# Performance work log

Hardware: AMD Instinct MI355X
Metric: run time of the kernel (lower is better)

Reference implementation:

```python
import jax, jax.numpy as jnp
import numpy as np

N_NODES = 100000


def gcn_conv(x, W, b, row, col, n):
    """PyG GCNConv: linear transform, then symmetric-normalized aggregation
    with self-loops (add_self_loops=True, normalize=True, bias=True)."""
    h = x @ W  # [N, F_out]
    e_ones = jnp.ones(row.shape[0], dtype=x.dtype)
    # in-degree of target nodes, +1 for the implicit self-loop
    deg = jax.ops.segment_sum(e_ones, col, num_segments=n) + 1.0
    dinv = jax.lax.rsqrt(deg)  # deg >= 1 always
    norm = dinv[row] * dinv[col]  # [E]
    msg = h[row] * norm[:, None]  # gather + scale, [E, F_out]
    agg = jax.ops.segment_sum(msg, col, num_segments=n)  # scatter-add to targets
    agg = agg + h * (dinv * dinv)[:, None]  # self-loop contribution
    return agg + b


def setup_inputs() -> dict:
    key = jax.random.key(0)
    k1, k2, k3, k4 = jax.random.split(key, 4)
    F_in, F_hid, F_out = 512, 64, 40
    E = 1_600_000
    x = jax.random.normal(k1, (N_NODES, F_in), dtype=jnp.float32)
    edge_index = jax.random.randint(k2, (2, E), 0, N_NODES, dtype=jnp.int64)
    # Glorot-ish scaling for weights
    W1 = jax.random.normal(k3, (F_in, F_hid), dtype=jnp.float32) * (1.0 / np.sqrt(F_in))
    W2 = jax.random.normal(k4, (F_hid, F_out), dtype=jnp.float32) * (1.0 / np.sqrt(F_hid))
    b1 = jnp.zeros((F_hid,), dtype=jnp.float32)
    b2 = jnp.zeros((F_out,), dtype=jnp.float32)
    return {"x": x, "edge_index": edge_index, "W1": W1, "b1": b1, "W2": W2, "b2": b2}


def reference(x, edge_index, W1, b1, W2, b2):
    n = x.shape[0]
    row, col = edge_index[0], edge_index[1]
    h = jax.nn.relu(gcn_conv(x, W1, b1, row, col, n))
    # dropout is identity in eval mode (training=False)
    h = gcn_conv(h, W2, b2, row, col, n)
    return jax.nn.log_softmax(h, axis=1)
```

## Files before the change

### kernel.cpp

```cpp
#include <hip/hip_runtime.h>
#include <math.h>


#define FIN 512
#define FHID 64
#define FOUT 40

#define BSH 8
#define BN 256
#define BCAP 5120
#define EPW 4096

typedef __attribute__((ext_vector_type(8))) short short8;
typedef __attribute__((ext_vector_type(4))) float f32x4;
typedef unsigned short ushort_t;
typedef unsigned int uint_t;

__device__ __forceinline__ ushort_t bf16_rn(float f) {
    union { float f; uint_t u; } v; v.f = f;
    uint_t r = v.u + 0x7FFF + ((v.u >> 16) & 1);
    return (ushort_t)(r >> 16);
}
__device__ __forceinline__ uint_t pack_bf16(float a, float b) {
    return (uint_t)bf16_rn(a) | ((uint_t)bf16_rn(b) << 16);
}
__device__ __forceinline__ float bf16_to_f(ushort_t u) {
    union { uint_t i; float f; } t; t.i = ((uint_t)u) << 16; return t.f;
}
__device__ __forceinline__ void acc8(float* acc, uint4 g, float nm) {
    acc[0] = fmaf(__uint_as_float(g.x << 16), nm, acc[0]);
    acc[1] = fmaf(__uint_as_float(g.x & 0xFFFF0000u), nm, acc[1]);
    acc[2] = fmaf(__uint_as_float(g.y << 16), nm, acc[2]);
    acc[3] = fmaf(__uint_as_float(g.y & 0xFFFF0000u), nm, acc[3]);
    acc[4] = fmaf(__uint_as_float(g.z << 16), nm, acc[4]);
    acc[5] = fmaf(__uint_as_float(g.z & 0xFFFF0000u), nm, acc[5]);
    acc[6] = fmaf(__uint_as_float(g.w << 16), nm, acc[6]);
    acc[7] = fmaf(__uint_as_float(g.w & 0xFFFF0000u), nm, acc[7]);
}

__global__ __launch_bounds__(256) void bucket_scatter_kernel(
    const int* __restrict__ row, const int* __restrict__ col,
    int* __restrict__ gcur, uint_t* __restrict__ stage, int E) {
    __shared__ uint_t cnt[512];
    __shared__ uint_t base[512];
    int tid = threadIdx.x;
    cnt[tid] = 0; cnt[tid + 256] = 0;
    __syncthreads();
    int e0 = blockIdx.x * EPW;
    int creg[16];
#pragma unroll
    for (int it = 0; it < 16; ++it) {
        int e = e0 + it * 256 + tid;
        creg[it] = (e < E) ? col[e] : -1;
        if (e < E) atomicAdd(&cnt[((uint_t)creg[it]) >> BSH], 1u);
    }
    __syncthreads();
    uint_t c0 = cnt[tid], c1 = cnt[tid + 256];
    base[tid] = c0 ? (uint_t)atomicAdd(&gcur[tid], (int)c0) : 0u;
    base[tid + 256] = c1 ? (uint_t)atomicAdd(&gcur[tid + 256], (int)c1) : 0u;
    __syncthreads();
    cnt[tid] = 0; cnt[tid + 256] = 0;
    __syncthreads();
#pragma unroll
    for (int it = 0; it < 16; ++it) {
        int e = e0 + it * 256 + tid;
        if (e < E) {
            int c = creg[it];
            int r = row[e];
            int b = c >> BSH;
            uint_t slot = base[b] + atomicAdd(&cnt[b], 1u);
            stage[(size_t)b * BCAP + slot] = ((uint_t)r << BSH) | (uint_t)(c & (BN - 1));
        }
    }
}

__global__ void scan2_kernel(int* __restrict__ bsums, int nb) {
    __shared__ int tmp[512];
    int tid = threadIdx.x;
    int v = (tid < nb) ? bsums[tid] : 0;
    tmp[tid] = v;
    __syncthreads();
    for (int off = 1; off < 512; off <<= 1) {
        int t = (tid >= off) ? tmp[tid - off] : 0;
        __syncthreads();
        tmp[tid] += t;
        __syncthreads();
    }
    if (tid < nb) bsums[tid] = tmp[tid] - v;
}

__global__ __launch_bounds__(256) void bucket_place_kernel(
    const int* __restrict__ gcur, const uint_t* __restrict__ stage,
    int* __restrict__ sSrc, int* __restrict__ deg, float* __restrict__ dinv,
    int* __restrict__ offs, int n) {
    __shared__ int lcnt[256];
    __shared__ int ltmp[256];
    __shared__ int lpos[256];
    int b = blockIdx.x, tid = threadIdx.x;
    int nodeBase = b << BSH;
    int bucketBase = gcur[b];
    int cnt = gcur[b + 1] - bucketBase;
    lcnt[tid] = 0;
    __syncthreads();
    const uint_t* sp = &stage[(size_t)b * BCAP];
    for (int i = tid; i < cnt; i += 256)
        atomicAdd(&lcnt[sp[i] & (BN - 1)], 1);
    __syncthreads();
    int v = lcnt[tid];
    ltmp[tid] = v;
    __syncthreads();
    for (int off = 1; off < 256; off <<= 1) {
        int t = (tid >= off) ? ltmp[tid - off] : 0;
        __syncthreads();
        ltmp[tid] += t;
        __syncthreads();
    }
    int gofs = bucketBase + ltmp[tid] - v;
    int node = nodeBase + tid;
    if (node < n) {
        deg[node] = v;
        dinv[node] = rsqrtf((float)v + 1.0f);
        offs[node] = gofs;
    }
    lpos[tid] = gofs;
    __syncthreads();
    for (int i = tid; i < cnt; i += 256) {
        uint_t w = sp[i];
        int pos = atomicAdd(&lpos[w & (BN - 1)], 1);
        sSrc[pos] = (int)(w >> BSH);
    }
}

__global__ void wprep_kernel(const float* __restrict__ W1, const float* __restrict__ W2,
                             ushort_t* __restrict__ Wt,
                             ushort_t* __restrict__ w2hi, ushort_t* __restrict__ w2lo) {
    int idx = blockIdx.x * 256 + threadIdx.x;
    if (idx < 32768) {
        int nrow = idx >> 9;
        int k = idx & 511;
        Wt[idx] = bf16_rn(W1[k * 64 + nrow]);
    } else if (idx < 32768 + 3072) {
        int i = idx - 32768;
        int j = i >> 6, k = i & 63;
        float w = (j < FOUT) ? W2[k * FOUT + j] : 0.f;
        ushort_t h = bf16_rn(w);
        w2hi[i] = h;
        w2lo[i] = bf16_rn(w - bf16_to_f(h));
    }
}

#define LDA 72
#define LDB 72
__global__ __launch_bounds__(256) void gemm1_kernel(
    const float* __restrict__ x, const ushort_t* __restrict__ Wt,
    ushort_t* __restrict__ h1b, int n) {
    __shared__ ushort_t lA[128 * LDA];
    __shared__ ushort_t lB[64 * LDB];

    int tid = threadIdx.x;
    int wave = tid >> 6, lane = tid & 63;
    int quad = lane >> 4, m16 = lane & 15;
    int node0 = blockIdx.x * 128;

    int r0 = tid >> 4, k4 = tid & 15;
    int nr0 = tid >> 3, seg = tid & 7;

    f32x4 zero = {0.f, 0.f, 0.f, 0.f};
    f32x4 acc[2][4];
#pragma unroll
    for (int mt = 0; mt < 2; ++mt)
#pragma unroll
        for (int nt = 0; nt < 4; ++nt) acc[mt][nt] = zero;

    float4 ra[8];
    uint4 rb[2];

#pragma unroll
    for (int i = 0; i < 8; ++i) {
        int node = node0 + r0 + i * 16;
        float4 v = make_float4(0.f, 0.f, 0.f, 0.f);
        if (node < n) v = *reinterpret_cast<const float4*>(&x[(size_t)node * FIN + k4 * 4]);
        ra[i] = v;
    }
#pragma unroll
    for (int i = 0; i < 2; ++i)
        rb[i] = *reinterpret_cast<const uint4*>(&Wt[(size_t)(nr0 + i * 32) * FIN + seg * 8]);

    for (int c = 0; c < 8; ++c) {
#pragma unroll
        for (int i = 0; i < 8; ++i)
            *reinterpret_cast<uint2*>(&lA[(r0 + i * 16) * LDA + k4 * 4]) =
                make_uint2(pack_bf16(ra[i].x, ra[i].y), pack_bf16(ra[i].z, ra[i].w));
#pragma unroll
        for (int i = 0; i < 2; ++i)
            *reinterpret_cast<uint4*>(&lB[(nr0 + i * 32) * LDB + seg * 8]) = rb[i];
        __syncthreads();

        if (c < 7) {
            int kc = (c + 1) * 64;
#pragma unroll
            for (int i = 0; i < 8; ++i) {
                int node = node0 + r0 + i * 16;
                float4 v = make_float4(0.f, 0.f, 0.f, 0.f);
                if (node < n)
                    v = *reinterpret_cast<const float4*>(&x[(size_t)node * FIN + kc + k4 * 4]);
                ra[i] = v;
            }
#pragma unroll
            for (int i = 0; i < 2; ++i)
                rb[i] = *reinterpret_cast<const uint4*>(
                    &Wt[(size_t)(nr0 + i * 32) * FIN + kc + seg * 8]);
        }

#pragma unroll
        for (int kk = 0; kk < 2; ++kk) {
            short8 a[2], b[4];
#pragma unroll
            for (int mt = 0; mt < 2; ++mt)
                a[mt] = *reinterpret_cast<const short8*>(
                    &lA[(wave * 32 + mt * 16 + m16) * LDA + kk * 32 + quad * 8]);
#pragma unroll
            for (int nt = 0; nt < 4; ++nt)
                b[nt] = *reinterpret_cast<const short8*>(
                    &lB[(nt * 16 + m16) * LDB + kk * 32 + quad * 8]);
#pragma unroll
            for (int mt = 0; mt < 2; ++mt)
#pragma unroll
                for (int nt = 0; nt < 4; ++nt)
                    acc[mt][nt] = __builtin_amdgcn_mfma_f32_16x16x32_bf16(
                        a[mt], b[nt], acc[mt][nt], 0, 0, 0);
        }
        __syncthreads();
    }

#pragma unroll
    for (int mt = 0; mt < 2; ++mt) {
#pragma unroll
        for (int reg = 0; reg < 4; ++reg) {
            int node = node0 + wave * 32 + mt * 16 + quad * 4 + reg;
            if (node < n) {
#pragma unroll
                for (int nt = 0; nt < 4; ++nt)
                    h1b[(size_t)node * 64 + nt * 16 + m16] = bf16_rn(acc[mt][nt][reg]);
            }
        }
    }
}

template <int MODE>
__global__ __launch_bounds__(256) void agg_kernel(
    const int* __restrict__ offs, const int* __restrict__ deg,
    const int* __restrict__ sSrc, const ushort_t* __restrict__ src,
    const float* __restrict__ dinv, const float* __restrict__ b1,
    ushort_t* __restrict__ dst, int n) {
    __shared__ float lacc[4][8 * 68];
    __shared__ float lb1[64];
    int tid = threadIdx.x;
    if (MODE == 0 && tid < 64) lb1[tid] = b1[tid];

    int wv = tid >> 6, lane = tid & 63;
    int e8 = lane >> 3, c = lane & 7;
    int node = blockIdx.x * 4 + wv;
    bool valid = node < n;
    int start = valid ? offs[node] : 0;
    int cnt = valid ? deg[node] : 0;

    float acc[8];
#pragma unroll
    for (int j = 0; j < 8; ++j) acc[j] = 0.f;

    for (int base = 0; base < cnt; base += 32) {
        int i0 = base + e8, i1 = i0 + 8, i2 = i0 + 16, i3 = i0 + 24;
        int s0 = (i0 < cnt) ? sSrc[start + i0] : 0;
        int s1 = (i1 < cnt) ? sSrc[start + i1] : 0;
        int s2 = (i2 < cnt) ? sSrc[start + i2] : 0;
        int s3 = (i3 < cnt) ? sSrc[start + i3] : 0;
        float nm0 = (i0 < cnt) ? dinv[s0] : 0.f;
        float nm1 = (i1 < cnt) ? dinv[s1] : 0.f;
        float nm2 = (i2 < cnt) ? dinv[s2] : 0.f;
        float nm3 = (i3 < cnt) ? dinv[s3] : 0.f;
        uint4 g0 = *reinterpret_cast<const uint4*>(&src[(size_t)s0 * 64 + c * 8]);
        uint4 g1 = *reinterpret_cast<const uint4*>(&src[(size_t)s1 * 64 + c * 8]);
        uint4 g2 = *reinterpret_cast<const uint4*>(&src[(size_t)s2 * 64 + c * 8]);
        uint4 g3 = *reinterpret_cast<const uint4*>(&src[(size_t)s3 * 64 + c * 8]);
        acc8(acc, g0, nm0);
        acc8(acc, g1, nm1);
        acc8(acc, g2, nm2);
        acc8(acc, g3, nm3);
    }

    {
        float* lw = &lacc[wv][e8 * 68 + c * 8];
        *reinterpret_cast<float4*>(lw) = make_float4(acc[0], acc[1], acc[2], acc[3]);
        *reinterpret_cast<float4*>(lw + 4) = make_float4(acc[4], acc[5], acc[6], acc[7]);
    }
    __syncthreads();

    if (valid) {
        float s = 0.f;
#pragma unroll
        for (int g = 0; g < 8; ++g) s += lacc[wv][g * 68 + lane];
        float di = dinv[node];
        float self = bf16_to_f(src[(size_t)node * 64 + lane]) * di;
        float v = (s + self) * di;
        if (MODE == 0) v = fmaxf(v + lb1[lane], 0.f);
        dst[(size_t)node * 64 + lane] = bf16_rn(v);
    }
}

#define LDC 72
__global__ __launch_bounds__(256) void gemm2sm_kernel(
    const ushort_t* __restrict__ A, const ushort_t* __restrict__ w2hi,
    const ushort_t* __restrict__ w2lo, const float* __restrict__ b2,
    float* __restrict__ out, int n) {
    __shared__ ushort_t lA[128 * LDC];
    __shared__ ushort_t lBh[48 * LDC];
    __shared__ ushort_t lBl[48 * LDC];

    int tid = threadIdx.x;
    int wave = tid >> 6, lane = tid & 63;
    int quad = lane >> 4, m16 = lane & 15;
    int node0 = blockIdx.x * 128;

    {
        int r = tid & 127, part = tid >> 7;
        int node = node0 + r;
        uint4 z = make_uint4(0u, 0u, 0u, 0u);
        const uint4* sp = reinterpret_cast<const uint4*>(&A[(size_t)node * 64 + part * 32]);
#pragma unroll
        for (int i = 0; i < 4; ++i) {
            uint4 v = (node < n) ? sp[i] : z;
            *reinterpret_cast<uint4*>(&lA[r * LDC + part * 32 + i * 8]) = v;
        }
    }
    for (int i = tid; i < 384; i += 256) {
        int row = i >> 3, seg = i & 7;
        *reinterpret_cast<uint4*>(&lBh[row * LDC + seg * 8]) =
            reinterpret_cast<const uint4*>(w2hi)[i];
        *reinterpret_cast<uint4*>(&lBl[row * LDC + seg * 8]) =
            reinterpret_cast<const uint4*>(w2lo)[i];
    }
    float rb2_0 = b2[m16];
    float rb2_1 = b2[16 + m16];
    float rb2_2 = (m16 < 8) ? b2[32 + m16] : 0.f;
    __syncthreads();

    f32x4 zero = {0.f, 0.f, 0.f, 0.f};
    f32x4 acc[2][3];
#pragma unroll
    for (int mt = 0; mt < 2; ++mt)
#pragma unroll
        for (int nt = 0; nt < 3; ++nt) acc[mt][nt] = zero;

#pragma unroll
    for (int kk = 0; kk < 2; ++kk) {
        short8 a[2], bh[3], bl[3];
#pragma unroll
        for (int mt = 0; mt < 2; ++mt)
            a[mt] = *reinterpret_cast<const short8*>(
                &lA[(wave * 32 + mt * 16 + m16) * LDC + kk * 32 + quad * 8]);
#pragma unroll
        for (int nt = 0; nt < 3; ++nt) {
            bh[nt] = *reinterpret_cast<const short8*>(
                &lBh[(nt * 16 + m16) * LDC + kk * 32 + quad * 8]);
            bl[nt] = *reinterpret_cast<const short8*>(
                &lBl[(nt * 16 + m16) * LDC + kk * 32 + quad * 8]);
        }
#pragma unroll
        for (int mt = 0; mt < 2; ++mt)
#pragma unroll
            for (int nt = 0; nt < 3; ++nt) {
                acc[mt][nt] = __builtin_amdgcn_mfma_f32_16x16x32_bf16(
                    a[mt], bh[nt], acc[mt][nt], 0, 0, 0);
                acc[mt][nt] = __builtin_amdgcn_mfma_f32_16x16x32_bf16(
                    a[mt], bl[nt], acc[mt][nt], 0, 0, 0);
            }
    }

    bool c2 = (m16 < 8);
#pragma unroll
    for (int mt = 0; mt < 2; ++mt) {
#pragma unroll
        for (int reg = 0; reg < 4; ++reg) {
            int node = node0 + wave * 32 + mt * 16 + quad * 4 + reg;
            float r0 = acc[mt][0][reg] + rb2_0;
            float r1 = acc[mt][1][reg] + rb2_1;
            float r2 = acc[mt][2][reg] + rb2_2;
            float pm = fmaxf(fmaxf(r0, r1), c2 ? r2 : -INFINITY);
#pragma unroll
            for (int mask = 1; mask <= 8; mask <<= 1)
                pm = fmaxf(pm, __shfl_xor(pm, mask));
            float s = expf(r0 - pm) + expf(r1 - pm) + (c2 ? expf(r2 - pm) : 0.f);
#pragma unroll
            for (int mask = 1; mask <= 8; mask <<= 1)
                s += __shfl_xor(s, mask);
            float ls = logf(s) + pm;
            if (node < n) {
                float* op = &out[(size_t)node * FOUT];
                op[m16] = r0 - ls;
                op[16 + m16] = r1 - ls;
                if (c2) op[32 + m16] = r2 - ls;
            }
        }
    }
}

extern "C" void kernel_launch(void* const* d_in, const int* in_sizes, int n_in,
                              void* d_out, int out_size, void* d_ws, size_t ws_size,
                              hipStream_t stream) {
    const float* x  = (const float*)d_in[0];
    const int*   ei = (const int*)d_in[1];
    const float* W1 = (const float*)d_in[2];
    const float* b1 = (const float*)d_in[3];
    const float* W2 = (const float*)d_in[4];
    const float* b2 = (const float*)d_in[5];
    float* out = (float*)d_out;

    int n = in_sizes[0] / FIN;
    int E = in_sizes[1] / 2;
    const int* row = ei;
    const int* col = ei + E;

    int* wsi = (int*)d_ws;
    const size_t NR = 100352;
    int*      deg   = wsi;
    float*    dinv  = (float*)(wsi + NR);
    int*      offs  = wsi + 2 * NR;
    int*      gcur  = wsi + 3 * NR;
    ushort_t* Wt    = (ushort_t*)(wsi + 3 * NR + 512);
    ushort_t* w2hi  = Wt + 64 * 512;
    ushort_t* w2lo  = w2hi + 48 * 64;
    uint_t*   stage = (uint_t*)(w2lo + 48 * 64);
    int*      sSrc  = (int*)(stage + (size_t)512 * BCAP);
    ushort_t* h1b   = (ushort_t*)(sSrc + (size_t)E);
    ushort_t* h1a   = h1b + (size_t)n * 64;
    ushort_t* Abuf  = h1b;

    int NBUCK = (n + BN - 1) >> BSH;
    int nwg1 = (E + EPW - 1) / EPW;

    hipMemsetAsync(gcur, 0, 512 * 4, stream);
    bucket_scatter_kernel<<<nwg1, 256, 0, stream>>>(row, col, gcur, stage, E);
    scan2_kernel<<<1, 512, 0, stream>>>(gcur, 512);
    bucket_place_kernel<<<NBUCK, 256, 0, stream>>>(gcur, stage, sSrc, deg, dinv, offs, n);

    wprep_kernel<<<140, 256, 0, stream>>>(W1, W2, Wt, w2hi, w2lo);

    gemm1_kernel<<<(n + 127) / 128, 256, 0, stream>>>(x, Wt, h1b, n);

    agg_kernel<0><<<(n + 3) / 4, 256, 0, stream>>>(offs, deg, sSrc, h1b, dinv, b1, h1a, n);

    agg_kernel<1><<<(n + 3) / 4, 256, 0, stream>>>(offs, deg, sSrc, h1a, dinv, b1, Abuf, n);

    gemm2sm_kernel<<<(n + 127) / 128, 256, 0, stream>>>(Abuf, w2hi, w2lo, b2, out, n);
}
```

Before: 461.7 us.

## Prescale features by dinv, drop per-edge dinv gather, two nodes per wave

Source-side degree normalization is folded into the producer: gemm1 multiplies its output rows by dinv, and the first aggregation epilogue multiplies its output by dinv again. The aggregation loop then only sums gathered rows, with no per-edge dinv gather or FMA. Padded edges point at a zeroed sentinel row n instead of being masked. Each wave now handles two nodes with 32 lanes apiece, and the epilogue writes packed bf16 pairs. This adds two small memsets and changes rounding slightly, because prescaled values are stored in bf16.

```diff
diff --git a/kernel.cpp b/kernel.cpp
--- a/kernel.cpp
+++ b/kernel.cpp
@@ -27,15 +27,15 @@
 __device__ __forceinline__ float bf16_to_f(ushort_t u) {
     union { uint_t i; float f; } t; t.i = ((uint_t)u) << 16; return t.f;
 }
-__device__ __forceinline__ void acc8(float* acc, uint4 g, float nm) {
-    acc[0] = fmaf(__uint_as_float(g.x << 16), nm, acc[0]);
-    acc[1] = fmaf(__uint_as_float(g.x & 0xFFFF0000u), nm, acc[1]);
-    acc[2] = fmaf(__uint_as_float(g.y << 16), nm, acc[2]);
-    acc[3] = fmaf(__uint_as_float(g.y & 0xFFFF0000u), nm, acc[3]);
-    acc[4] = fmaf(__uint_as_float(g.z << 16), nm, acc[4]);
-    acc[5] = fmaf(__uint_as_float(g.z & 0xFFFF0000u), nm, acc[5]);
-    acc[6] = fmaf(__uint_as_float(g.w << 16), nm, acc[6]);
-    acc[7] = fmaf(__uint_as_float(g.w & 0xFFFF0000u), nm, acc[7]);
+__device__ __forceinline__ void add8(float* acc, uint4 g) {
+    acc[0] += __uint_as_float(g.x << 16);
+    acc[1] += __uint_as_float(g.x & 0xFFFF0000u);
+    acc[2] += __uint_as_float(g.y << 16);
+    acc[3] += __uint_as_float(g.y & 0xFFFF0000u);
+    acc[4] += __uint_as_float(g.z << 16);
+    acc[5] += __uint_as_float(g.z & 0xFFFF0000u);
+    acc[6] += __uint_as_float(g.w << 16);
+    acc[7] += __uint_as_float(g.w & 0xFFFF0000u);
 }
 
 __global__ __launch_bounds__(256) void bucket_scatter_kernel(
@@ -153,7 +153,7 @@
 #define LDB 72
 __global__ __launch_bounds__(256) void gemm1_kernel(
     const float* __restrict__ x, const ushort_t* __restrict__ Wt,
-    ushort_t* __restrict__ h1b, int n) {
+    const float* __restrict__ dinv, ushort_t* __restrict__ h1b, int n) {
     __shared__ ushort_t lA[128 * LDA];
     __shared__ ushort_t lB[64 * LDB];
 
@@ -239,9 +239,11 @@
         for (int reg = 0; reg < 4; ++reg) {
             int node = node0 + wave * 32 + mt * 16 + quad * 4 + reg;
             if (node < n) {
+                float di = dinv[node];
 #pragma unroll
                 for (int nt = 0; nt < 4; ++nt)
-                    h1b[(size_t)node * 64 + nt * 16 + m16] = bf16_rn(acc[mt][nt][reg]);
+                    h1b[(size_t)node * 64 + nt * 16 + m16] =
+                        bf16_rn(acc[mt][nt][reg] * di);
             }
         }
     }
@@ -253,14 +255,17 @@
     const int* __restrict__ sSrc, const ushort_t* __restrict__ src,
     const float* __restrict__ dinv, const float* __restrict__ b1,
     ushort_t* __restrict__ dst, int n) {
-    __shared__ float lacc[4][8 * 68];
+    __shared__ float lacc[8][4 * 68];
     __shared__ float lb1[64];
     int tid = threadIdx.x;
     if (MODE == 0 && tid < 64) lb1[tid] = b1[tid];
 
     int wv = tid >> 6, lane = tid & 63;
-    int e8 = lane >> 3, c = lane & 7;
-    int node = blockIdx.x * 4 + wv;
+    int half = lane >> 5;
+    int l32 = lane & 31;
+    int e4 = l32 >> 3, c = l32 & 7;
+    int slot = wv * 2 + half;
+    int node = blockIdx.x * 8 + slot;
     bool valid = node < n;
     int start = valid ? offs[node] : 0;
     int cnt = valid ? deg[node] : 0;
@@ -269,42 +274,50 @@
 #pragma unroll
     for (int j = 0; j < 8; ++j) acc[j] = 0.f;
 
-    for (int base = 0; base < cnt; base += 32) {
-        int i0 = base + e8, i1 = i0 + 8, i2 = i0 + 16, i3 = i0 + 24;
-        int s0 = (i0 < cnt) ? sSrc[start + i0] : 0;
-        int s1 = (i1 < cnt) ? sSrc[start + i1] : 0;
-        int s2 = (i2 < cnt) ? sSrc[start + i2] : 0;
-        int s3 = (i3 < cnt) ? sSrc[start + i3] : 0;
-        float nm0 = (i0 < cnt) ? dinv[s0] : 0.f;
-        float nm1 = (i1 < cnt) ? dinv[s1] : 0.f;
-        float nm2 = (i2 < cnt) ? dinv[s2] : 0.f;
-        float nm3 = (i3 < cnt) ? dinv[s3] : 0.f;
+    for (int base = 0; base < cnt; base += 16) {
+        int i0 = base + e4, i1 = i0 + 4, i2 = i0 + 8, i3 = i0 + 12;
+        int s0 = (i0 < cnt) ? sSrc[start + i0] : n;
+        int s1 = (i1 < cnt) ? sSrc[start + i1] : n;
+        int s2 = (i2 < cnt) ? sSrc[start + i2] : n;
+        int s3 = (i3 < cnt) ? sSrc[start + i3] : n;
         uint4 g0 = *reinterpret_cast<const uint4*>(&src[(size_t)s0 * 64 + c * 8]);
         uint4 g1 = *reinterpret_cast<const uint4*>(&src[(size_t)s1 * 64 + c * 8]);
         uint4 g2 = *reinterpret_cast<const uint4*>(&src[(size_t)s2 * 64 + c * 8]);
         uint4 g3 = *reinterpret_cast<const uint4*>(&src[(size_t)s3 * 64 + c * 8]);
-        acc8(acc, g0, nm0);
-        acc8(acc, g1, nm1);
-        acc8(acc, g2, nm2);
-        acc8(acc, g3, nm3);
+        add8(acc, g0);
+        add8(acc, g1);
+        add8(acc, g2);
+        add8(acc, g3);
     }
 
     {
-        float* lw = &lacc[wv][e8 * 68 + c * 8];
+        float* lw = &lacc[slot][e4 * 68 + c * 8];
         *reinterpret_cast<float4*>(lw) = make_float4(acc[0], acc[1], acc[2], acc[3]);
         *reinterpret_cast<float4*>(lw + 4) = make_float4(acc[4], acc[5], acc[6], acc[7]);
     }
     __syncthreads();
 
-    if (valid) {
-        float s = 0.f;
-#pragma unroll
-        for (int g = 0; g < 8; ++g) s += lacc[wv][g * 68 + lane];
-        float di = dinv[node];
-        float self = bf16_to_f(src[(size_t)node * 64 + lane]) * di;
-        float v = (s + self) * di;
-        if (MODE == 0) v = fmaxf(v + lb1[lane], 0.f);
-        dst[(size_t)node * 64 + lane] = bf16_rn(v);
+    int s = tid >> 5;
+    int fp = tid & 31;
+    int enode = blockIdx.x * 8 + s;
+    if (enode < n) {
+        float sum0 = 0.f, sum1 = 0.f;
+#pragma unroll
+        for (int g = 0; g < 4; ++g) {
+            sum0 += lacc[s][g * 68 + fp * 2];
+            sum1 += lacc[s][g * 68 + fp * 2 + 1];
+        }
+        float di = dinv[enode];
+        uint_t sv = *reinterpret_cast<const uint_t*>(&src[(size_t)enode * 64 + fp * 2]);
+        float self0 = __uint_as_float(sv << 16);
+        float self1 = __uint_as_float(sv & 0xFFFF0000u);
+        float v0 = (sum0 + self0) * di;
+        float v1 = (sum1 + self1) * di;
+        if (MODE == 0) {
+            v0 = fmaxf(v0 + lb1[fp * 2], 0.f) * di;
+            v1 = fmaxf(v1 + lb1[fp * 2 + 1], 0.f) * di;
+        }
+        *reinterpret_cast<uint_t*>(&dst[(size_t)enode * 64 + fp * 2]) = pack_bf16(v0, v1);
     }
 }
 
@@ -433,24 +446,26 @@
     uint_t*   stage = (uint_t*)(w2lo + 48 * 64);
     int*      sSrc  = (int*)(stage + (size_t)512 * BCAP);
     ushort_t* h1b   = (ushort_t*)(sSrc + (size_t)E);
-    ushort_t* h1a   = h1b + (size_t)n * 64;
+    ushort_t* h1a   = h1b + (size_t)(n + 1) * 64;
     ushort_t* Abuf  = h1b;
 
     int NBUCK = (n + BN - 1) >> BSH;
     int nwg1 = (E + EPW - 1) / EPW;
 
     hipMemsetAsync(gcur, 0, 512 * 4, stream);
+    hipMemsetAsync(h1b + (size_t)n * 64, 0, 128, stream);
+    hipMemsetAsync(h1a + (size_t)n * 64, 0, 128, stream);
     bucket_scatter_kernel<<<nwg1, 256, 0, stream>>>(row, col, gcur, stage, E);
     scan2_kernel<<<1, 512, 0, stream>>>(gcur, 512);
     bucket_place_kernel<<<NBUCK, 256, 0, stream>>>(gcur, stage, sSrc, deg, dinv, offs, n);
 
     wprep_kernel<<<140, 256, 0, stream>>>(W1, W2, Wt, w2hi, w2lo);
 
-    gemm1_kernel<<<(n + 127) / 128, 256, 0, stream>>>(x, Wt, h1b, n);
-
-    agg_kernel<0><<<(n + 3) / 4, 256, 0, stream>>>(offs, deg, sSrc, h1b, dinv, b1, h1a, n);
-
-    agg_kernel<1><<<(n + 3) / 4, 256, 0, stream>>>(offs, deg, sSrc, h1a, dinv, b1, Abuf, n);
+    gemm1_kernel<<<(n + 127) / 128, 256, 0, stream>>>(x, Wt, dinv, h1b, n);
+
+    agg_kernel<0><<<(n + 7) / 8, 256, 0, stream>>>(offs, deg, sSrc, h1b, dinv, b1, h1a, n);
+
+    agg_kernel<1><<<(n + 7) / 8, 256, 0, stream>>>(offs, deg, sSrc, h1a, dinv, b1, Abuf, n);
 
     gemm2sm_kernel<<<(n + 127) / 128, 256, 0, stream>>>(Abuf, w2hi, w2lo, b2, out, n);
 }
```

After: 445.9 us. 1.04x faster.
